# Kernel optimization log

Measured on AMD Instinct MI355X. Metric: run time of the kernel, lower is better.

Reference implementation:

```python
import jax, jax.numpy as jnp
import numpy as np

EMBED = 768
HEADS = 12
D_K = EMBED // HEADS  # 64


def setup_inputs() -> dict:
    key = jax.random.key(0)
    ks = jax.random.split(key, 9)
    w_scale = EMBED ** -0.5
    inp = {
        "x": jax.random.normal(ks[0], (128, 256, 1, EMBED), dtype=jnp.float32),
        "Wq": jax.random.normal(ks[1], (EMBED, EMBED), dtype=jnp.float32) * w_scale,
        "bq": jax.random.normal(ks[2], (EMBED,), dtype=jnp.float32) * 0.02,
        "Wk": jax.random.normal(ks[3], (EMBED, EMBED), dtype=jnp.float32) * w_scale,
        "bk": jax.random.normal(ks[4], (EMBED,), dtype=jnp.float32) * 0.02,
        "Wv": jax.random.normal(ks[5], (EMBED, EMBED), dtype=jnp.float32) * w_scale,
        "bv": jax.random.normal(ks[6], (EMBED,), dtype=jnp.float32) * 0.02,
        "Wo": jax.random.normal(ks[7], (EMBED, EMBED), dtype=jnp.float32) * w_scale,
        "bo": jax.random.normal(ks[8], (EMBED,), dtype=jnp.float32) * 0.02,
    }
    return inp


def reference(x, Wq, bq, Wk, bk, Wv, bv, Wo, bo):
    # x: (n_rows r, n_cols i/j, batch n, embed)
    R, C, B, E = x.shape
    H, Dk = HEADS, D_K
    # tied-row scaling: d_k^{-1/2} / sqrt(n_rows)
    scaling = (Dk ** -0.5) / np.sqrt(R).astype(np.float32)

    q = (x @ Wq.T + bq).reshape(R, C, B, H, Dk) * scaling
    k = (x @ Wk.T + bk).reshape(R, C, B, H, Dk)
    v = (x @ Wv.T + bv).reshape(R, C, B, H, Dk)

    # scores summed over rows r and head dim d -> (h, n, i, j)
    scores = jnp.einsum('rinhd,rjnhd->hnij', q, k)
    probs = jax.nn.softmax(scores, axis=-1)  # dropout p=0 -> identity

    # shared attention applied per row
    c = jnp.einsum('hnij,rjnhd->rinhd', probs, v).reshape(R, C, B, E)
    out = c @ Wo.T + bo
    return (out, probs)
```

## Files before the change

### kernel.cpp

```cpp
#include <hip/hip_runtime.h>
#include <math.h>

typedef short bf16x8 __attribute__((ext_vector_type(8)));
typedef float f32x4 __attribute__((ext_vector_type(4)));
typedef unsigned short ushort8 __attribute__((ext_vector_type(8)));
typedef unsigned short ushort4v __attribute__((ext_vector_type(4)));

constexpr int R = 128, Cc = 256, E = 768, H = 12;
constexpr int M = R * Cc;
constexpr size_t TOK = (size_t)M * E;

__device__ __forceinline__ unsigned short f2b(float f) {
  unsigned int u = __float_as_uint(f);
  u += 0x7fff + ((u >> 16) & 1);
  return (unsigned short)(u >> 16);
}

__device__ __forceinline__ void ldst16(const unsigned short* g, unsigned short* l) {
  __builtin_amdgcn_global_load_lds(
      (const __attribute__((address_space(1))) unsigned int*)g,
      (__attribute__((address_space(3))) unsigned int*)l, 16, 0, 0);
}

__global__ __launch_bounds__(256) void cvt_bf16(const float* __restrict__ in,
                                                unsigned short* __restrict__ out,
                                                int n8) {
  int i = blockIdx.x * 256 + threadIdx.x;
  if (i >= n8) return;
  const float4* p = (const float4*)in;
  float4 a = p[2 * i], b = p[2 * i + 1];
  ushort8 o;
  o[0] = f2b(a.x); o[1] = f2b(a.y); o[2] = f2b(a.z); o[3] = f2b(a.w);
  o[4] = f2b(b.x); o[5] = f2b(b.y); o[6] = f2b(b.z); o[7] = f2b(b.w);
  ((ushort8*)out)[i] = o;
}

__device__ __forceinline__ void gemm128(const unsigned short* __restrict__ A, int lda,
                                        const unsigned short* __restrict__ B, int ldb,
                                        int K, unsigned short* As, unsigned short* Bs,
                                        int wv, int ln, int wm, int wn,
                                        f32x4 (&acc)[4][4]) {
  const int srow = ln >> 2, scol = (ln & 3) * 8;
  for (int k0 = 0; k0 < K; k0 += 32) {
    __syncthreads();
#pragma unroll
    for (int t = 0; t < 2; ++t) {
      const int ch = wv * 2 + t;
      const int row = ch * 16 + srow;
      ldst16(A + (size_t)row * lda + k0 + scol, As + ch * 512 + ln * 8);
      ldst16(B + (size_t)row * ldb + k0 + scol, Bs + ch * 512 + ln * 8);
    }
    __syncthreads();
    bf16x8 a[4], b[4];
#pragma unroll
    for (int i = 0; i < 4; ++i)
      a[i] = *(const bf16x8*)(As + (wm + i * 16 + (ln & 15)) * 32 + (ln >> 4) * 8);
#pragma unroll
    for (int j = 0; j < 4; ++j)
      b[j] = *(const bf16x8*)(Bs + (wn + j * 16 + (ln & 15)) * 32 + (ln >> 4) * 8);
#pragma unroll
    for (int i = 0; i < 4; ++i)
#pragma unroll
      for (int j = 0; j < 4; ++j)
        acc[i][j] = __builtin_amdgcn_mfma_f32_16x16x32_bf16(a[i], b[j], acc[i][j], 0, 0, 0);
  }
}

__global__ __launch_bounds__(256) void qkv_proj(
    const unsigned short* __restrict__ A, const unsigned short* __restrict__ B,
    const float* __restrict__ bq, const float* __restrict__ bk,
    const float* __restrict__ bv, unsigned short* __restrict__ q2,
    unsigned short* __restrict__ k2, unsigned short* __restrict__ v3, float scaling) {
  __shared__ unsigned short As[128 * 32];
  __shared__ unsigned short Bs[128 * 32];
  const int tid = threadIdx.x, wv = tid >> 6, ln = tid & 63;
  const unsigned p = blockIdx.x + blockIdx.y * 18;
  const unsigned l = (p & 7) * 576 + (p >> 3);
  const int bx = l % 18, by = l / 18;
  const int n0 = bx * 128, m0 = by * 128;
  const int wm = (wv & 1) * 64, wn = (wv >> 1) * 64;
  f32x4 acc[4][4] = {};
  gemm128(A + (size_t)m0 * 768, 768, B + (size_t)n0 * 768, 768, 768,
          As, Bs, wv, ln, wm, wn, acc);

  const int region = bx / 6;
  const float* bias = region == 0 ? bq : (region == 1 ? bk : bv);
  const float sc = region == 0 ? scaling : 1.0f;
  const int nq0 = n0 - region * 768;
#pragma unroll
  for (int j = 0; j < 4; ++j) {
    const int np = nq0 + wn + j * 16 + (ln & 15);
    const int h = np >> 6, d = np & 63;
    const float bn = bias[np];
#pragma unroll
    for (int i = 0; i < 4; ++i) {
      const int mb = m0 + wm + i * 16 + (ln >> 4) * 4;
      if (region < 2) {
        unsigned short* dst = region == 0 ? q2 : k2;
#pragma unroll
        for (int r = 0; r < 4; ++r) {
          const int m = mb + r;
          const int ic = m & 255, rr = m >> 8;
          dst[(size_t)h * 2097152 + (size_t)ic * 8192 + rr * 64 + d] =
              f2b((acc[i][j][r] + bn) * sc);
        }
      } else {
        const int jc = mb & 255, rr = mb >> 8;
        ushort4v o;
#pragma unroll
        for (int r = 0; r < 4; ++r) o[r] = f2b(acc[i][j][r] + bn);
        *(ushort4v*)(v3 + (size_t)h * 2097152 + ((size_t)rr * 64 + d) * 256 + jc) = o;
      }
    }
  }
}

__global__ __launch_bounds__(256) void qk_gemm(const unsigned short* __restrict__ q2,
                                               const unsigned short* __restrict__ k2,
                                               float* __restrict__ Sp) {
  __shared__ unsigned short As[128 * 32];
  __shared__ unsigned short Bs[128 * 32];
  const int tid = threadIdx.x, wv = tid >> 6, ln = tid & 63;
  const int i0 = (blockIdx.x & 1) * 128, j0 = (blockIdx.x >> 1) * 128;
  const int h = blockIdx.y, kc = blockIdx.z;
  const int wm = (wv & 1) * 64, wn = (wv >> 1) * 64;
  f32x4 acc[4][4] = {};
  const unsigned short* Ap = q2 + (size_t)h * 2097152 + (size_t)i0 * 8192 + kc * 1024;
  const unsigned short* Bp = k2 + (size_t)h * 2097152 + (size_t)j0 * 8192 + kc * 1024;
  gemm128(Ap, 8192, Bp, 8192, 1024, As, Bs, wv, ln, wm, wn, acc);
  float* out = Sp + ((size_t)kc * H + h) * 65536;
#pragma unroll
  for (int j = 0; j < 4; ++j) {
    const int jj = j0 + wn + j * 16 + (ln & 15);
#pragma unroll
    for (int i = 0; i < 4; ++i)
#pragma unroll
      for (int r = 0; r < 4; ++r) {
        const int ii = i0 + wm + i * 16 + (ln >> 4) * 4 + r;
        out[(size_t)ii * 256 + jj] = acc[i][j][r];
      }
  }
}

__global__ __launch_bounds__(256) void softmax_k(const float* __restrict__ Sp,
                                                 float* __restrict__ P,
                                                 unsigned short* __restrict__ Pb) {
  const int row = blockIdx.x, j = threadIdx.x;
  const size_t stride = (size_t)H * Cc * Cc;
  const size_t base = (size_t)row * Cc + j;
  float s = 0.f;
#pragma unroll
  for (int c = 0; c < 8; ++c) s += Sp[base + c * stride];
  float m = s;
#pragma unroll
  for (int o = 32; o > 0; o >>= 1) m = fmaxf(m, __shfl_xor(m, o));
  __shared__ float sm[4], ss[4];
  const int wid = j >> 6, lane = j & 63;
  if (lane == 0) sm[wid] = m;
  __syncthreads();
  m = fmaxf(fmaxf(sm[0], sm[1]), fmaxf(sm[2], sm[3]));
  float e = expf(s - m);
  float t = e;
#pragma unroll
  for (int o = 32; o > 0; o >>= 1) t += __shfl_xor(t, o);
  if (lane == 0) ss[wid] = t;
  __syncthreads();
  t = ss[0] + ss[1] + ss[2] + ss[3];
  const float p = e / t;
  P[base] = p;
  Pb[base] = f2b(p);
}

__global__ __launch_bounds__(256) void pv_gemm(const unsigned short* __restrict__ P,
                                               const unsigned short* __restrict__ V,
                                               unsigned short* __restrict__ Co) {
  __shared__ unsigned short As[128 * 32];
  __shared__ unsigned short Bs[128 * 32];
  const int tid = threadIdx.x, wv = tid >> 6, ln = tid & 63;
  const unsigned p = blockIdx.x + blockIdx.y * 128;
  const unsigned l = (p & 7) * 192 + (p >> 3);
  const int bx = l & 127, h = l >> 7;
  const int i0 = (bx & 1) * 128, n0 = (bx >> 1) * 128;
  const int wm = (wv & 1) * 64, wn = (wv >> 1) * 64;
  f32x4 acc[4][4] = {};
  const unsigned short* Ap = P + (size_t)h * 65536 + (size_t)i0 * 256;
  const unsigned short* Bp = V + (size_t)h * 2097152 + (size_t)n0 * 256;
  gemm128(Ap, 256, Bp, 256, 256, As, Bs, wv, ln, wm, wn, acc);
#pragma unroll
  for (int j = 0; j < 4; ++j) {
    const int n = n0 + wn + j * 16 + (ln & 15);
    const int rr = n >> 6, d = n & 63;
#pragma unroll
    for (int i = 0; i < 4; ++i)
#pragma unroll
      for (int r = 0; r < 4; ++r) {
        const int ii = i0 + wm + i * 16 + (ln >> 4) * 4 + r;
        Co[((size_t)rr * 256 + ii) * 768 + h * 64 + d] = f2b(acc[i][j][r]);
      }
  }
}

__global__ __launch_bounds__(256) void o_proj(const unsigned short* __restrict__ A,
                                              const unsigned short* __restrict__ B,
                                              const float* __restrict__ bias,
                                              float* __restrict__ Y) {
  __shared__ unsigned short As[128 * 32];
  __shared__ unsigned short Bs[128 * 32];
  const int tid = threadIdx.x, wv = tid >> 6, ln = tid & 63;
  const unsigned p = blockIdx.x + blockIdx.y * 6;
  const unsigned l = (p & 7) * 192 + (p >> 3);
  const int bx = l % 6, by = l / 6;
  const int n0 = bx * 128, m0 = by * 128;
  const int wm = (wv & 1) * 64, wn = (wv >> 1) * 64;
  f32x4 acc[4][4] = {};
  gemm128(A + (size_t)m0 * 768, 768, B + (size_t)n0 * 768, 768, 768,
          As, Bs, wv, ln, wm, wn, acc);
#pragma unroll
  for (int j = 0; j < 4; ++j) {
    const int n = n0 + wn + j * 16 + (ln & 15);
    const float bn = bias[n];
#pragma unroll
    for (int i = 0; i < 4; ++i)
#pragma unroll
      for (int r = 0; r < 4; ++r) {
        const int m = m0 + wm + i * 16 + (ln >> 4) * 4 + r;
        Y[(size_t)m * 768 + n] = acc[i][j][r] + bn;
      }
  }
}

extern "C" void kernel_launch(void* const* d_in, const int* in_sizes, int n_in,
                              void* d_out, int out_size, void* d_ws, size_t ws_size,
                              hipStream_t stream) {
  const float* x  = (const float*)d_in[0];
  const float* Wq = (const float*)d_in[1];
  const float* bq = (const float*)d_in[2];
  const float* Wk = (const float*)d_in[3];
  const float* bk = (const float*)d_in[4];
  const float* Wv = (const float*)d_in[5];
  const float* bv = (const float*)d_in[6];
  const float* Wo = (const float*)d_in[7];
  const float* bo = (const float*)d_in[8];
  float* out = (float*)d_out;
  float* probs = out + TOK;

  char* ws = (char*)d_ws;
  unsigned short* x_bf  = (unsigned short*)(ws);
  unsigned short* q2    = (unsigned short*)(ws + 50331648);
  unsigned short* k2    = (unsigned short*)(ws + 100663296);
  unsigned short* v3    = (unsigned short*)(ws + 150994944);
  unsigned short* Wq_bf = (unsigned short*)(ws + 201326592);
  unsigned short* Wk_bf = Wq_bf + 589824;
  unsigned short* Wv_bf = Wk_bf + 589824;
  unsigned short* Wo_bf = Wv_bf + 589824;
  float* S_part         = (float*)(ws);
  unsigned short* P_bf  = (unsigned short*)(ws + 25165824);
  unsigned short* c_bf  = q2;

  const float scaling = 0.125f / sqrtf(128.f);

  cvt_bf16<<<12288, 256, 0, stream>>>(x, x_bf, 3145728);
  cvt_bf16<<<288, 256, 0, stream>>>(Wq, Wq_bf, 73728);
  cvt_bf16<<<288, 256, 0, stream>>>(Wk, Wk_bf, 73728);
  cvt_bf16<<<288, 256, 0, stream>>>(Wv, Wv_bf, 73728);
  cvt_bf16<<<288, 256, 0, stream>>>(Wo, Wo_bf, 73728);

  qkv_proj<<<dim3(18, 256), 256, 0, stream>>>(x_bf, Wq_bf, bq, bk, bv,
                                              q2, k2, v3, scaling);

  qk_gemm<<<dim3(4, H, 8), 256, 0, stream>>>(q2, k2, S_part);
  softmax_k<<<H * Cc, 256, 0, stream>>>(S_part, probs, P_bf);
  pv_gemm<<<dim3(128, H), 256, 0, stream>>>(P_bf, v3, c_bf);

  o_proj<<<dim3(6, 256), 256, 0, stream>>>(c_bf, Wo_bf, bo, out);
}
```

Measured before the change: 545.9 us.

## Triple-buffer GEMM LDS staging with swizzle and merge weight conversion kernels

```diff
diff --git a/kernel.cpp b/kernel.cpp
--- a/kernel.cpp
+++ b/kernel.cpp
@@ -35,34 +35,76 @@
   ((ushort8*)out)[i] = o;
 }
 
+__global__ __launch_bounds__(256) void cvt_w4(const float* __restrict__ W0,
+                                              const float* __restrict__ W1,
+                                              const float* __restrict__ W2,
+                                              const float* __restrict__ W3,
+                                              unsigned short* __restrict__ out) {
+  const int region = blockIdx.x / 288;
+  const int i = (blockIdx.x % 288) * 256 + threadIdx.x;
+  if (i >= 73728) return;
+  const float* src = region == 0 ? W0 : (region == 1 ? W1 : (region == 2 ? W2 : W3));
+  const float4* p = (const float4*)src;
+  float4 a = p[2 * i], b = p[2 * i + 1];
+  ushort8 o;
+  o[0] = f2b(a.x); o[1] = f2b(a.y); o[2] = f2b(a.z); o[3] = f2b(a.w);
+  o[4] = f2b(b.x); o[5] = f2b(b.y); o[6] = f2b(b.z); o[7] = f2b(b.w);
+  ((ushort8*)(out + (size_t)region * 589824))[i] = o;
+}
+
+__device__ __forceinline__ void stage32(const unsigned short* __restrict__ A, int lda,
+                                        const unsigned short* __restrict__ B, int ldb,
+                                        int k0, unsigned short* As, unsigned short* Bs,
+                                        int tid) {
+  const int row = tid >> 2;
+  const int g = ((tid & 3) ^ ((row >> 1) & 3)) * 8;
+  ldst16(A + (size_t)row * lda + k0 + g, As + tid * 8);
+  ldst16(A + (size_t)(row + 64) * lda + k0 + g, As + 2048 + tid * 8);
+  ldst16(B + (size_t)row * ldb + k0 + g, Bs + tid * 8);
+  ldst16(B + (size_t)(row + 64) * ldb + k0 + g, Bs + 2048 + tid * 8);
+}
+
 __device__ __forceinline__ void gemm128(const unsigned short* __restrict__ A, int lda,
                                         const unsigned short* __restrict__ B, int ldb,
                                         int K, unsigned short* As, unsigned short* Bs,
-                                        int wv, int ln, int wm, int wn,
+                                        int tid, int ln, int wm, int wn,
                                         f32x4 (&acc)[4][4]) {
-  const int srow = ln >> 2, scol = (ln & 3) * 8;
-  for (int k0 = 0; k0 < K; k0 += 32) {
-    __syncthreads();
-#pragma unroll
-    for (int t = 0; t < 2; ++t) {
-      const int ch = wv * 2 + t;
-      const int row = ch * 16 + srow;
-      ldst16(A + (size_t)row * lda + k0 + scol, As + ch * 512 + ln * 8);
-      ldst16(B + (size_t)row * ldb + k0 + scol, Bs + ch * 512 + ln * 8);
+  const int nt = K >> 5;
+  stage32(A, lda, B, ldb, 0, As, Bs, tid);
+  stage32(A, lda, B, ldb, 32, As + 4096, Bs + 4096, tid);
+  const int rc = ((ln >> 4) ^ ((ln >> 1) & 3)) * 8;
+  for (int t = 0; t < nt; ++t) {
+    if (t + 1 < nt) {
+      asm volatile("s_waitcnt vmcnt(4)" ::: "memory");
+    } else {
+      asm volatile("s_waitcnt vmcnt(0)" ::: "memory");
     }
-    __syncthreads();
+    __builtin_amdgcn_sched_barrier(0);
+    __builtin_amdgcn_s_barrier();
+    __builtin_amdgcn_sched_barrier(0);
+    if (t + 2 < nt) {
+      const int s2 = ((t + 2) % 3) * 4096;
+      stage32(A, lda, B, ldb, (t + 2) << 5, As + s2, Bs + s2, tid);
+    }
+    const int s = (t % 3) * 4096;
+    const unsigned short* Ab = As + s;
+    const unsigned short* Bb = Bs + s;
     bf16x8 a[4], b[4];
 #pragma unroll
     for (int i = 0; i < 4; ++i)
-      a[i] = *(const bf16x8*)(As + (wm + i * 16 + (ln & 15)) * 32 + (ln >> 4) * 8);
+      a[i] = *(const bf16x8*)(Ab + (wm + i * 16 + (ln & 15)) * 32 + rc);
 #pragma unroll
     for (int j = 0; j < 4; ++j)
-      b[j] = *(const bf16x8*)(Bs + (wn + j * 16 + (ln & 15)) * 32 + (ln >> 4) * 8);
+      b[j] = *(const bf16x8*)(Bb + (wn + j * 16 + (ln & 15)) * 32 + rc);
+    asm volatile("s_waitcnt lgkmcnt(0)" ::: "memory");
+    __builtin_amdgcn_sched_barrier(0);
+    __builtin_amdgcn_s_setprio(1);
 #pragma unroll
     for (int i = 0; i < 4; ++i)
 #pragma unroll
       for (int j = 0; j < 4; ++j)
         acc[i][j] = __builtin_amdgcn_mfma_f32_16x16x32_bf16(a[i], b[j], acc[i][j], 0, 0, 0);
+    __builtin_amdgcn_s_setprio(0);
   }
 }
 
@@ -71,8 +113,8 @@
     const float* __restrict__ bq, const float* __restrict__ bk,
     const float* __restrict__ bv, unsigned short* __restrict__ q2,
     unsigned short* __restrict__ k2, unsigned short* __restrict__ v3, float scaling) {
-  __shared__ unsigned short As[128 * 32];
-  __shared__ unsigned short Bs[128 * 32];
+  __shared__ unsigned short As[3 * 4096];
+  __shared__ unsigned short Bs[3 * 4096];
   const int tid = threadIdx.x, wv = tid >> 6, ln = tid & 63;
   const unsigned p = blockIdx.x + blockIdx.y * 18;
   const unsigned l = (p & 7) * 576 + (p >> 3);
@@ -81,7 +123,7 @@
   const int wm = (wv & 1) * 64, wn = (wv >> 1) * 64;
   f32x4 acc[4][4] = {};
   gemm128(A + (size_t)m0 * 768, 768, B + (size_t)n0 * 768, 768, 768,
-          As, Bs, wv, ln, wm, wn, acc);
+          As, Bs, tid, ln, wm, wn, acc);
 
   const int region = bx / 6;
   const float* bias = region == 0 ? bq : (region == 1 ? bk : bv);
@@ -118,8 +160,8 @@
 __global__ __launch_bounds__(256) void qk_gemm(const unsigned short* __restrict__ q2,
                                                const unsigned short* __restrict__ k2,
                                                float* __restrict__ Sp) {
-  __shared__ unsigned short As[128 * 32];
-  __shared__ unsigned short Bs[128 * 32];
+  __shared__ unsigned short As[3 * 4096];
+  __shared__ unsigned short Bs[3 * 4096];
   const int tid = threadIdx.x, wv = tid >> 6, ln = tid & 63;
   const int i0 = (blockIdx.x & 1) * 128, j0 = (blockIdx.x >> 1) * 128;
   const int h = blockIdx.y, kc = blockIdx.z;
@@ -127,7 +169,7 @@
   f32x4 acc[4][4] = {};
   const unsigned short* Ap = q2 + (size_t)h * 2097152 + (size_t)i0 * 8192 + kc * 1024;
   const unsigned short* Bp = k2 + (size_t)h * 2097152 + (size_t)j0 * 8192 + kc * 1024;
-  gemm128(Ap, 8192, Bp, 8192, 1024, As, Bs, wv, ln, wm, wn, acc);
+  gemm128(Ap, 8192, Bp, 8192, 1024, As, Bs, tid, ln, wm, wn, acc);
   float* out = Sp + ((size_t)kc * H + h) * 65536;
 #pragma unroll
   for (int j = 0; j < 4; ++j) {
@@ -174,8 +216,8 @@
 __global__ __launch_bounds__(256) void pv_gemm(const unsigned short* __restrict__ P,
                                                const unsigned short* __restrict__ V,
                                                unsigned short* __restrict__ Co) {
-  __shared__ unsigned short As[128 * 32];
-  __shared__ unsigned short Bs[128 * 32];
+  __shared__ unsigned short As[3 * 4096];
+  __shared__ unsigned short Bs[3 * 4096];
   const int tid = threadIdx.x, wv = tid >> 6, ln = tid & 63;
   const unsigned p = blockIdx.x + blockIdx.y * 128;
   const unsigned l = (p & 7) * 192 + (p >> 3);
@@ -185,7 +227,7 @@
   f32x4 acc[4][4] = {};
   const unsigned short* Ap = P + (size_t)h * 65536 + (size_t)i0 * 256;
   const unsigned short* Bp = V + (size_t)h * 2097152 + (size_t)n0 * 256;
-  gemm128(Ap, 256, Bp, 256, 256, As, Bs, wv, ln, wm, wn, acc);
+  gemm128(Ap, 256, Bp, 256, 256, As, Bs, tid, ln, wm, wn, acc);
 #pragma unroll
   for (int j = 0; j < 4; ++j) {
     const int n = n0 + wn + j * 16 + (ln & 15);
@@ -204,8 +246,8 @@
                                               const unsigned short* __restrict__ B,
                                               const float* __restrict__ bias,
                                               float* __restrict__ Y) {
-  __shared__ unsigned short As[128 * 32];
-  __shared__ unsigned short Bs[128 * 32];
+  __shared__ unsigned short As[3 * 4096];
+  __shared__ unsigned short Bs[3 * 4096];
   const int tid = threadIdx.x, wv = tid >> 6, ln = tid & 63;
   const unsigned p = blockIdx.x + blockIdx.y * 6;
   const unsigned l = (p & 7) * 192 + (p >> 3);
@@ -214,7 +256,7 @@
   const int wm = (wv & 1) * 64, wn = (wv >> 1) * 64;
   f32x4 acc[4][4] = {};
   gemm128(A + (size_t)m0 * 768, 768, B + (size_t)n0 * 768, 768, 768,
-          As, Bs, wv, ln, wm, wn, acc);
+          As, Bs, tid, ln, wm, wn, acc);
 #pragma unroll
   for (int j = 0; j < 4; ++j) {
     const int n = n0 + wn + j * 16 + (ln & 15);
@@ -250,9 +292,7 @@
   unsigned short* k2    = (unsigned short*)(ws + 100663296);
   unsigned short* v3    = (unsigned short*)(ws + 150994944);
   unsigned short* Wq_bf = (unsigned short*)(ws + 201326592);
-  unsigned short* Wk_bf = Wq_bf + 589824;
-  unsigned short* Wv_bf = Wk_bf + 589824;
-  unsigned short* Wo_bf = Wv_bf + 589824;
+  unsigned short* Wo_bf = Wq_bf + 3 * 589824;
   float* S_part         = (float*)(ws);
   unsigned short* P_bf  = (unsigned short*)(ws + 25165824);
   unsigned short* c_bf  = q2;
@@ -260,10 +300,7 @@
   const float scaling = 0.125f / sqrtf(128.f);
 
   cvt_bf16<<<12288, 256, 0, stream>>>(x, x_bf, 3145728);
-  cvt_bf16<<<288, 256, 0, stream>>>(Wq, Wq_bf, 73728);
-  cvt_bf16<<<288, 256, 0, stream>>>(Wk, Wk_bf, 73728);
-  cvt_bf16<<<288, 256, 0, stream>>>(Wv, Wv_bf, 73728);
-  cvt_bf16<<<288, 256, 0, stream>>>(Wo, Wo_bf, 73728);
+  cvt_w4<<<1152, 256, 0, stream>>>(Wq, Wk, Wv, Wo, Wq_bf);
 
   qkv_proj<<<dim3(18, 256), 256, 0, stream>>>(x_bf, Wq_bf, bq, bk, bv,
                                               q2, k2, v3, scaling);
```

Result: faster. 506.4 us (-7.2%).
